# Performance work log

Measured on AMD Instinct MI355X. Metric: run time of the kernel, lower is better.

## Reference

```python
import jax, jax.numpy as jnp
import numpy as np

N = 50000       # num nodes
F_NODE = 8      # node_features
T_IN = 8        # num_timestamps_in (A3TGCN periods)
T_OUT = 4       # num_timestamps_out
HID = 16        # A3TGCN out_channels (hard-coded in module)
E = 800000      # num edges


def setup_inputs() -> dict:
    key = jax.random.key(0)
    ks = jax.random.split(key, 12)
    f32 = jnp.float32
    x = jax.random.normal(ks[0], (N, F_NODE, T_IN), dtype=f32)
    edge_index = jax.random.randint(ks[1], (2, E), 0, N)

    def w(k, shape):
        return (jax.random.normal(k, shape, dtype=f32) * 0.1)

    return {
        "x": x,
        "edge_index": edge_index,
        "attention": w(ks[2], (T_IN,)),
        "Wz": w(ks[3], (F_NODE, HID)), "bz": jnp.zeros((HID,), f32),
        "Lz_w": w(ks[4], (2 * HID, HID)), "Lz_b": jnp.zeros((HID,), f32),
        "Wr": w(ks[5], (F_NODE, HID)), "br": jnp.zeros((HID,), f32),
        "Lr_w": w(ks[6], (2 * HID, HID)), "Lr_b": jnp.zeros((HID,), f32),
        "Wh": w(ks[7], (F_NODE, HID)), "bh": jnp.zeros((HID,), f32),
        "Lh_w": w(ks[8], (2 * HID, HID)), "Lh_b": jnp.zeros((HID,), f32),
        "W_out": w(ks[9], (HID, F_NODE)), "b_out": jnp.zeros((F_NODE,), f32),
    }


def _gcn_norms(src, dst):
    # PyG gcn_norm: add self loops (weight 1), symmetric D^-1/2 (A+I) D^-1/2
    deg = jax.ops.segment_sum(jnp.ones((E,), jnp.float32), dst, num_segments=N) + 1.0
    dinv = jax.lax.rsqrt(deg)
    return dinv[src] * dinv[dst], dinv * dinv  # per-edge norm, self-loop norm


def _gcn(X, W, b, src, dst, norm_e, norm_self):
    xw = X @ W                                        # [N, HID]
    agg = jax.ops.segment_sum(xw[src] * norm_e[:, None], dst, num_segments=N)
    return agg + norm_self[:, None] * xw + b


def reference(x, edge_index, attention,
              Wz, bz, Lz_w, Lz_b,
              Wr, br, Lr_w, Lr_b,
              Wh, bh, Lh_w, Lh_b,
              W_out, b_out):
    src, dst = edge_index[0], edge_index[1]
    norm_e, norm_self = _gcn_norms(src, dst)
    probs = jax.nn.softmax(attention)                 # attention over periods

    def tgcn_cell(Xp, H):
        # GRU with GCNConv-based gates (TGCN)
        Z = jax.nn.sigmoid(
            jnp.concatenate([_gcn(Xp, Wz, bz, src, dst, norm_e, norm_self), H], axis=1) @ Lz_w + Lz_b)
        R = jax.nn.sigmoid(
            jnp.concatenate([_gcn(Xp, Wr, br, src, dst, norm_e, norm_self), H], axis=1) @ Lr_w + Lr_b)
        H_t = jnp.tanh(
            jnp.concatenate([_gcn(Xp, Wh, bh, src, dst, norm_e, norm_self), H * R], axis=1) @ Lh_w + Lh_b)
        return Z * H + (1.0 - Z) * H_t

    def a3tgcn(x_cur):
        xs = jnp.transpose(x_cur, (2, 0, 1))          # [T_IN, N, F]
        def step(carry, inp):
            H, H_acc = carry
            Xp, p = inp
            H = tgcn_cell(Xp, H)
            return (H, H_acc + p * H), None
        init = (jnp.zeros((N, HID), x_cur.dtype), jnp.zeros((N, HID), x_cur.dtype))
        (_, H_acc), _ = jax.lax.scan(step, init, (xs, probs))
        return H_acc

    outs = []
    for _ in range(T_OUT):
        h = jax.nn.relu(a3tgcn(x)) @ W_out + b_out    # [N, F]
        h = h[:, :, None]                              # [N, F, 1]
        x = jnp.concatenate([x[:, :, 1:], h], axis=2)  # slide window
        outs.append(h)
    return jnp.concatenate(outs, axis=2)               # [N, F, T_OUT]
```

## Files before the change

kernel.cpp:

```cpp
#include <hip/hip_runtime.h>

#define NN 50000
#define NE 800000
#define N8 (8*NN)
#define CAP 64

__device__ __forceinline__ float sigmoidf_(float x){ return 1.0f/(1.0f+__expf(-x)); }
__device__ __forceinline__ float tanhfast_(float x){ return 1.0f - 2.0f/(__expf(2.0f*x)+1.0f); }

__global__ void k_zero_fold(int* __restrict__ cnt, const float* __restrict__ att,
    const float* __restrict__ Wz, const float* __restrict__ bz,
    const float* __restrict__ Lzw, const float* __restrict__ Lzb,
    const float* __restrict__ Wr, const float* __restrict__ br,
    const float* __restrict__ Lrw, const float* __restrict__ Lrb,
    const float* __restrict__ Wh, const float* __restrict__ bh,
    const float* __restrict__ Lhw, const float* __restrict__ Lhb,
    const float* __restrict__ Wo, const float* __restrict__ bo,
    float* __restrict__ fold){
    if(blockIdx.x < 196){
        cnt[blockIdx.x*256 + threadIdx.x] = 0;
        return;
    }
    int tid = threadIdx.x;
    const float* Ws[3]  = {Wz, Wr, Wh};
    const float* bs[3]  = {bz, br, bh};
    const float* Ls[3]  = {Lzw, Lrw, Lhw};
    const float* Lbs[3] = {Lzb, Lrb, Lhb};
    if(tid < 48){
        int g = tid >> 4, j = tid & 15;
        const float* W = Ws[g]; const float* L = Ls[g];
        float c = Lbs[g][j];
        for(int k = 0; k < 16; ++k) c += bs[g][k] * L[k*16 + j];
        fold[1280 + g*16 + j] = c;
        for(int f = 0; f < 8; ++f){
            float m = 0.f;
            for(int k = 0; k < 16; ++k) m += W[f*16 + k] * L[k*16 + j];
            fold[j*28 + g*8 + f] = m;
        }
    }
    for(int idx = tid; idx < 768; idx += 256){
        int g = idx >> 8, rr = idx & 255, i = rr >> 4, j = rr & 15;
        fold[448 + j*52 + g*16 + i] = Ls[g][(16 + i)*16 + j];
    }
    for(int idx = tid; idx < 128; idx += 256) fold[1328 + idx] = Wo[idx];
    if(tid < 8) fold[1456 + tid] = bo[tid];
    if(tid == 0){
        float mx = att[0];
        for(int k = 1; k < 8; ++k) mx = fmaxf(mx, att[k]);
        float den = 0.f, ex[8];
        for(int k = 0; k < 8; ++k){ ex[k] = __expf(att[k] - mx); den += ex[k]; }
        for(int k = 0; k < 8; ++k) fold[1464 + k] = ex[k] / den;
    }
}

__global__ void k_hist(const int* __restrict__ ei, int* __restrict__ cnt,
                       int* __restrict__ rank){
    int e = blockIdx.x*256 + threadIdx.x;
    rank[e] = atomicAdd(&cnt[ei[NE + e]], 1);
}

__global__ void k_scatter_xscale(const int* __restrict__ ei, const int* __restrict__ rank,
                                 int* __restrict__ csr, const float* __restrict__ x,
                                 const int* __restrict__ cnt, float* __restrict__ xs){
    if(blockIdx.x < 3125){
        int e = blockIdx.x*256 + threadIdx.x;
        int r = rank[e];
        if(r < CAP) csr[(size_t)ei[NE + e]*CAP + r] = ei[e];
    } else {
        int idx = (blockIdx.x - 3125)*256 + threadIdx.x;
        int n = idx >> 4;
        const float4* x4 = (const float4*)x;
        float4 v = x4[idx];
        float d = rsqrtf((float)cnt[n] + 1.0f);
        v.x *= d; v.y *= d; v.z *= d; v.w *= d;
        ((float4*)xs)[idx] = v;
    }
}

__global__ __launch_bounds__(256) void k_gather_x2(
    const int* __restrict__ cnt, const int* __restrict__ csr,
    const float* __restrict__ xs, float* __restrict__ Pall){
    int lane = threadIdx.x & 63;
    int n = blockIdx.x*4 + (threadIdx.x >> 6);
    int g = lane >> 4;
    int q = lane & 15;
    int cn = cnt[n];
    int deg = cn < CAP ? cn : CAP;
    const int* row = csr + (size_t)n*CAP;
    const float4* xs4 = (const float4*)xs;

    float4 a0, a1, a2, a3;
    if(g == 0){ a0 = xs4[(size_t)n*16 + q]; }
    else      { a0.x = a0.y = a0.z = a0.w = 0.f; }
    a1.x = a1.y = a1.z = a1.w = 0.f;
    a2 = a1; a3 = a1;

    int it = 0;
    for(; it + 16 <= deg; it += 16){
        int ka = it + g;
        int s0 = row[ka], s1 = row[ka+4], s2 = row[ka+8], s3 = row[ka+12];
        float4 v0 = xs4[(size_t)s0*16 + q];
        float4 v1 = xs4[(size_t)s1*16 + q];
        float4 v2 = xs4[(size_t)s2*16 + q];
        float4 v3 = xs4[(size_t)s3*16 + q];
        a0.x += v0.x; a0.y += v0.y; a0.z += v0.z; a0.w += v0.w;
        a1.x += v1.x; a1.y += v1.y; a1.z += v1.z; a1.w += v1.w;
        a2.x += v2.x; a2.y += v2.y; a2.z += v2.z; a2.w += v2.w;
        a3.x += v3.x; a3.y += v3.y; a3.z += v3.z; a3.w += v3.w;
    }
    for(int k = it + g; k < deg; k += 4){
        float4 v = xs4[(size_t)row[k]*16 + q];
        a0.x += v.x; a0.y += v.y; a0.z += v.z; a0.w += v.w;
    }
    a0.x += a1.x + a2.x + a3.x;
    a0.y += a1.y + a2.y + a3.y;
    a0.z += a1.z + a2.z + a3.z;
    a0.w += a1.w + a2.w + a3.w;

    a0.x += __shfl_xor(a0.x, 16); a0.y += __shfl_xor(a0.y, 16);
    a0.z += __shfl_xor(a0.z, 16); a0.w += __shfl_xor(a0.w, 16);
    a0.x += __shfl_xor(a0.x, 32); a0.y += __shfl_xor(a0.y, 32);
    a0.z += __shfl_xor(a0.z, 32); a0.w += __shfl_xor(a0.w, 32);

    if(g == 0){
        float dn = rsqrtf((float)cn + 1.0f);
        float a[4] = {a0.x, a0.y, a0.z, a0.w};
        #pragma unroll
        for(int m = 0; m < 4; ++m){
            int r = q*4 + m;
            int f = r >> 3, t = r & 7;
            Pall[(size_t)t*N8 + n*8 + f] = dn * a[m];
        }
    }
}

template<int TOUT>
__global__ __launch_bounds__(256) void k_cell_t(
    const float* __restrict__ Pall, float* __restrict__ Ph_all,
    const float* __restrict__ fold, const int* __restrict__ cnt,
    const int* __restrict__ csr, float* __restrict__ out,
    const float* __restrict__ hs_in, float* __restrict__ hs_out){
    __shared__ float s[1472];
    __shared__ float xch[256];
    for(int k = threadIdx.x; k < 1472; k += 256) s[k] = fold[k];
    __syncthreads();

    int tid = threadIdx.x;
    int j = tid & 15;
    int nb = tid & 240;
    int n = blockIdx.x*16 + (tid >> 4);
    int cn = cnt[n];
    float dn = rsqrtf((float)cn + 1.0f);

    float u7[8];
    if(TOUT > 0){
        int f = j & 7, g = j >> 3;
        int deg = cn < CAP ? cn : CAP;
        const int* row = csr + (size_t)n*CAP;
        float ga = 0.f, gb = 0.f;
        int k = g;
        for(; k + 4 <= deg; k += 4){
            ga += hs_in[row[k]*8 + f];
            gb += hs_in[row[k+2]*8 + f];
        }
        if(k < deg){ ga += hs_in[row[k]*8 + f]; k += 2; }
        if(k < deg){ gb += hs_in[row[k]*8 + f]; }
        ga += gb;
        ga += __shfl_xor(ga, 8);
        float uh = dn * (ga + hs_in[n*8 + f]);
        if(j < 8){
            xch[nb + j] = uh;
            Ph_all[(size_t)(TOUT-1)*N8 + n*8 + j] = uh;
        }
        *(float4*)&u7[0] = *(const float4*)&xch[nb + 0];
        *(float4*)&u7[4] = *(const float4*)&xch[nb + 4];
    }

    const float* Mrow = s + j*28;
    const float* Lrow = s + 448 + j*52;
    float mw[24];
    #pragma unroll
    for(int k = 0; k < 6; ++k) *(float4*)&mw[k*4] = *(const float4*)&Mrow[k*4];
    float lw[48];
    #pragma unroll
    for(int k = 0; k < 12; ++k) *(float4*)&lw[k*4] = *(const float4*)&Lrow[k*4];
    float cz = s[1280 + j], cr = s[1296 + j], ch = s[1312 + j];

    float Hown = 0.f, Acc = 0.f;

    #pragma unroll
    for(int st = 0; st < 8; ++st){
        const int t = TOUT + st;
        float u[8];
        if(TOUT > 0 && st == 7){
            #pragma unroll
            for(int f = 0; f < 8; ++f) u[f] = u7[f];
        } else {
            const float* Pu = (t < 8) ? (Pall + (size_t)t*N8 + n*8)
                                      : (Ph_all + (size_t)(t - 8)*N8 + n*8);
            const float4* Pu4 = (const float4*)Pu;
            float4 b0 = Pu4[0], b1 = Pu4[1];
            u[0]=b0.x; u[1]=b0.y; u[2]=b0.z; u[3]=b0.w;
            u[4]=b1.x; u[5]=b1.y; u[6]=b1.z; u[7]=b1.w;
        }

        float Hf[16];
        xch[tid] = Hown;
        *(float4*)&Hf[0]  = *(const float4*)&xch[nb + 0];
        *(float4*)&Hf[4]  = *(const float4*)&xch[nb + 4];
        *(float4*)&Hf[8]  = *(const float4*)&xch[nb + 8];
        *(float4*)&Hf[12] = *(const float4*)&xch[nb + 12];

        float az = cz, ar = cr;
        #pragma unroll
        for(int f = 0; f < 8; ++f){ az += u[f]*mw[f]; ar += u[f]*mw[8+f]; }
        #pragma unroll
        for(int i = 0; i < 16; ++i){ az += Hf[i]*lw[i]; ar += Hf[i]*lw[16+i]; }
        float Z = sigmoidf_(az);
        float R = sigmoidf_(ar);

        float HRf[16];
        xch[tid] = Hown*R;
        *(float4*)&HRf[0]  = *(const float4*)&xch[nb + 0];
        *(float4*)&HRf[4]  = *(const float4*)&xch[nb + 4];
        *(float4*)&HRf[8]  = *(const float4*)&xch[nb + 8];
        *(float4*)&HRf[12] = *(const float4*)&xch[nb + 12];

        float ah = ch;
        #pragma unroll
        for(int f = 0; f < 8; ++f) ah += u[f]*mw[16+f];
        #pragma unroll
        for(int i = 0; i < 16; ++i) ah += HRf[i]*lw[32+i];
        float ht = tanhfast_(ah);
        Hown = Z*Hown + (1.0f - Z)*ht;
        Acc += s[1464 + st]*Hown;
    }

    float rf[16];
    xch[tid] = Acc > 0.f ? Acc : 0.f;
    *(float4*)&rf[0]  = *(const float4*)&xch[nb + 0];
    *(float4*)&rf[4]  = *(const float4*)&xch[nb + 4];
    *(float4*)&rf[8]  = *(const float4*)&xch[nb + 8];
    *(float4*)&rf[12] = *(const float4*)&xch[nb + 12];
    if(j < 8){
        int f = j;
        float o = s[1456 + f];
        #pragma unroll
        for(int jj = 0; jj < 16; ++jj) o += rf[jj] * s[1328 + jj*8 + f];
        out[(size_t)n*32 + f*4 + TOUT] = o;
        if(TOUT < 3) hs_out[n*8 + f] = dn * o;
    }
}

extern "C" void kernel_launch(void* const* d_in, const int* in_sizes, int n_in,
                              void* d_out, int out_size, void* d_ws, size_t ws_size,
                              hipStream_t stream){
    const float* x   = (const float*)d_in[0];
    const int*   ei  = (const int*)  d_in[1];
    const float* att = (const float*)d_in[2];
    const float* Wz  = (const float*)d_in[3];  const float* bz  = (const float*)d_in[4];
    const float* Lzw = (const float*)d_in[5];  const float* Lzb = (const float*)d_in[6];
    const float* Wr  = (const float*)d_in[7];  const float* br  = (const float*)d_in[8];
    const float* Lrw = (const float*)d_in[9];  const float* Lrb = (const float*)d_in[10];
    const float* Wh  = (const float*)d_in[11]; const float* bh  = (const float*)d_in[12];
    const float* Lhw = (const float*)d_in[13]; const float* Lhb = (const float*)d_in[14];
    const float* Wo  = (const float*)d_in[15]; const float* bo  = (const float*)d_in[16];
    float* out = (float*)d_out;

    char* w = (char*)d_ws;
    int*   cnt  = (int*)  (w);
    int*   csr  = (int*)  (w + (size_t)50176*4);
    float* fold = (float*)(w + (size_t)3250176*4);
    float* xs   = (float*)(w + (size_t)3251712*4);
    float* Pall = (float*)(w + (size_t)6451712*4);
    int*   rank = (int*)Pall;
    float* Ph   = xs;
    float* hs0  = xs + 1200000;
    float* hs1  = xs + 1600000;

    dim3 b(256);
    k_zero_fold<<<197, b, 0, stream>>>(cnt, att, Wz, bz, Lzw, Lzb, Wr, br, Lrw, Lrb,
                                       Wh, bh, Lhw, Lhb, Wo, bo, fold);
    k_hist<<<3125, b, 0, stream>>>(ei, cnt, rank);
    k_scatter_xscale<<<6250, b, 0, stream>>>(ei, rank, csr, x, cnt, xs);
    k_gather_x2<<<12500, b, 0, stream>>>(cnt, csr, xs, Pall);

    k_cell_t<0><<<3125, b, 0, stream>>>(Pall, Ph, fold, cnt, csr, out, hs1, hs0);
    k_cell_t<1><<<3125, b, 0, stream>>>(Pall, Ph, fold, cnt, csr, out, hs0, hs1);
    k_cell_t<2><<<3125, b, 0, stream>>>(Pall, Ph, fold, cnt, csr, out, hs1, hs0);
    k_cell_t<3><<<3125, b, 0, stream>>>(Pall, Ph, fold, cnt, csr, out, hs0, hs1);
}
```

Baseline: 312.8 us.

## Process two nodes per thread group in GRU cell kernel and fuse CSR build

The cell kernel now handles two nodes per 16-lane group, so each loaded weight is reused across both nodes and the number of blocks is halved. The H exchange through shared memory packs both nodes as float2. Separately, the histogram and CSR scatter are merged into one atomic-rank-and-write kernel, and the x scaling gets its own launch, which drops the rank array round trip. In exchange the cell kernel uses more registers, which may lower occupancy, and the fused build makes the CSR slot order depend on atomic timing.

```diff
diff --git a/kernel.cpp b/kernel.cpp
--- a/kernel.cpp
+++ b/kernel.cpp
@@ -53,28 +53,23 @@
     }
 }
 
-__global__ void k_hist(const int* __restrict__ ei, int* __restrict__ cnt,
-                       int* __restrict__ rank){
+__global__ void k_build(const int* __restrict__ ei, int* __restrict__ cnt,
+                        int* __restrict__ csr){
     int e = blockIdx.x*256 + threadIdx.x;
-    rank[e] = atomicAdd(&cnt[ei[NE + e]], 1);
-}
-
-__global__ void k_scatter_xscale(const int* __restrict__ ei, const int* __restrict__ rank,
-                                 int* __restrict__ csr, const float* __restrict__ x,
-                                 const int* __restrict__ cnt, float* __restrict__ xs){
-    if(blockIdx.x < 3125){
-        int e = blockIdx.x*256 + threadIdx.x;
-        int r = rank[e];
-        if(r < CAP) csr[(size_t)ei[NE + e]*CAP + r] = ei[e];
-    } else {
-        int idx = (blockIdx.x - 3125)*256 + threadIdx.x;
-        int n = idx >> 4;
-        const float4* x4 = (const float4*)x;
-        float4 v = x4[idx];
-        float d = rsqrtf((float)cnt[n] + 1.0f);
-        v.x *= d; v.y *= d; v.z *= d; v.w *= d;
-        ((float4*)xs)[idx] = v;
-    }
+    int s = ei[e], d = ei[NE + e];
+    int r = atomicAdd(&cnt[d], 1);
+    if(r < CAP) csr[(size_t)d*CAP + r] = s;
+}
+
+__global__ void k_xscale(const float* __restrict__ x, const int* __restrict__ cnt,
+                         float* __restrict__ xs){
+    int idx = blockIdx.x*256 + threadIdx.x;
+    int n = idx >> 4;
+    const float4* x4 = (const float4*)x;
+    float4 v = x4[idx];
+    float d = rsqrtf((float)cnt[n] + 1.0f);
+    v.x *= d; v.y *= d; v.z *= d; v.w *= d;
+    ((float4*)xs)[idx] = v;
 }
 
 __global__ __launch_bounds__(256) void k_gather_x2(
@@ -141,39 +136,56 @@
     const int* __restrict__ csr, float* __restrict__ out,
     const float* __restrict__ hs_in, float* __restrict__ hs_out){
     __shared__ float s[1472];
-    __shared__ float xch[256];
+    __shared__ float xch[16*36];
     for(int k = threadIdx.x; k < 1472; k += 256) s[k] = fold[k];
     __syncthreads();
 
     int tid = threadIdx.x;
     int j = tid & 15;
-    int nb = tid & 240;
-    int n = blockIdx.x*16 + (tid >> 4);
-    int cn = cnt[n];
-    float dn = rsqrtf((float)cn + 1.0f);
-
-    float u7[8];
+    int grp = tid >> 4;
+    float2* xb = (float2*)&xch[grp*36];
+    const float4* xb4 = (const float4*)xb;
+    int n0 = blockIdx.x*32 + grp;
+    int n1 = n0 + 16;
+    bool v1 = (n1 < NN);
+    int n1c = v1 ? n1 : NN-1;
+    int c0 = cnt[n0], c1 = cnt[n1c];
+    float dn0 = rsqrtf((float)c0 + 1.f), dn1 = rsqrtf((float)c1 + 1.f);
+
+    float u7x[8], u7y[8];
     if(TOUT > 0){
-        int f = j & 7, g = j >> 3;
-        int deg = cn < CAP ? cn : CAP;
-        const int* row = csr + (size_t)n*CAP;
-        float ga = 0.f, gb = 0.f;
-        int k = g;
-        for(; k + 4 <= deg; k += 4){
-            ga += hs_in[row[k]*8 + f];
-            gb += hs_in[row[k+2]*8 + f];
-        }
-        if(k < deg){ ga += hs_in[row[k]*8 + f]; k += 2; }
-        if(k < deg){ gb += hs_in[row[k]*8 + f]; }
-        ga += gb;
-        ga += __shfl_xor(ga, 8);
-        float uh = dn * (ga + hs_in[n*8 + f]);
+        int f = j & 7, g2 = j >> 3;
+        int d0 = c0 < CAP ? c0 : CAP;
+        int d1 = c1 < CAP ? c1 : CAP;
+        const int* r0 = csr + (size_t)n0*CAP;
+        const int* r1 = csr + (size_t)n1c*CAP;
+        float a0 = 0.f, b0 = 0.f, a1 = 0.f, b1 = 0.f;
+        int k = g2;
+        for(; k + 4 <= d0; k += 4){
+            a0 += hs_in[r0[k]*8 + f];
+            b0 += hs_in[r0[k+2]*8 + f];
+        }
+        if(k < d0){ a0 += hs_in[r0[k]*8 + f]; k += 2; }
+        if(k < d0){ b0 += hs_in[r0[k]*8 + f]; }
+        k = g2;
+        for(; k + 4 <= d1; k += 4){
+            a1 += hs_in[r1[k]*8 + f];
+            b1 += hs_in[r1[k+2]*8 + f];
+        }
+        if(k < d1){ a1 += hs_in[r1[k]*8 + f]; k += 2; }
+        if(k < d1){ b1 += hs_in[r1[k]*8 + f]; }
+        a0 += b0; a1 += b1;
+        a0 += __shfl_xor(a0, 8);
+        a1 += __shfl_xor(a1, 8);
+        float uh0 = dn0*(a0 + hs_in[n0*8 + f]);
+        float uh1 = dn1*(a1 + hs_in[n1c*8 + f]);
         if(j < 8){
-            xch[nb + j] = uh;
-            Ph_all[(size_t)(TOUT-1)*N8 + n*8 + j] = uh;
-        }
-        *(float4*)&u7[0] = *(const float4*)&xch[nb + 0];
-        *(float4*)&u7[4] = *(const float4*)&xch[nb + 4];
+            xb[j] = make_float2(uh0, uh1);
+            Ph_all[(size_t)(TOUT-1)*N8 + n0*8 + j] = uh0;
+            if(v1) Ph_all[(size_t)(TOUT-1)*N8 + n1*8 + j] = uh1;
+        }
+        #pragma unroll
+        for(int ff = 0; ff < 8; ++ff){ float2 t2 = xb[ff]; u7x[ff] = t2.x; u7y[ff] = t2.y; }
     }
 
     const float* Mrow = s + j*28;
@@ -186,69 +198,78 @@
     for(int k = 0; k < 12; ++k) *(float4*)&lw[k*4] = *(const float4*)&Lrow[k*4];
     float cz = s[1280 + j], cr = s[1296 + j], ch = s[1312 + j];
 
-    float Hown = 0.f, Acc = 0.f;
+    float2 H = make_float2(0.f, 0.f), Acc = make_float2(0.f, 0.f);
 
     #pragma unroll
     for(int st = 0; st < 8; ++st){
         const int t = TOUT + st;
-        float u[8];
+        float ux[8], uy[8];
         if(TOUT > 0 && st == 7){
             #pragma unroll
-            for(int f = 0; f < 8; ++f) u[f] = u7[f];
+            for(int f = 0; f < 8; ++f){ ux[f] = u7x[f]; uy[f] = u7y[f]; }
         } else {
-            const float* Pu = (t < 8) ? (Pall + (size_t)t*N8 + n*8)
-                                      : (Ph_all + (size_t)(t - 8)*N8 + n*8);
-            const float4* Pu4 = (const float4*)Pu;
-            float4 b0 = Pu4[0], b1 = Pu4[1];
-            u[0]=b0.x; u[1]=b0.y; u[2]=b0.z; u[3]=b0.w;
-            u[4]=b1.x; u[5]=b1.y; u[6]=b1.z; u[7]=b1.w;
-        }
-
-        float Hf[16];
-        xch[tid] = Hown;
-        *(float4*)&Hf[0]  = *(const float4*)&xch[nb + 0];
-        *(float4*)&Hf[4]  = *(const float4*)&xch[nb + 4];
-        *(float4*)&Hf[8]  = *(const float4*)&xch[nb + 8];
-        *(float4*)&Hf[12] = *(const float4*)&xch[nb + 12];
-
-        float az = cz, ar = cr;
-        #pragma unroll
-        for(int f = 0; f < 8; ++f){ az += u[f]*mw[f]; ar += u[f]*mw[8+f]; }
-        #pragma unroll
-        for(int i = 0; i < 16; ++i){ az += Hf[i]*lw[i]; ar += Hf[i]*lw[16+i]; }
-        float Z = sigmoidf_(az);
-        float R = sigmoidf_(ar);
-
-        float HRf[16];
-        xch[tid] = Hown*R;
-        *(float4*)&HRf[0]  = *(const float4*)&xch[nb + 0];
-        *(float4*)&HRf[4]  = *(const float4*)&xch[nb + 4];
-        *(float4*)&HRf[8]  = *(const float4*)&xch[nb + 8];
-        *(float4*)&HRf[12] = *(const float4*)&xch[nb + 12];
-
-        float ah = ch;
-        #pragma unroll
-        for(int f = 0; f < 8; ++f) ah += u[f]*mw[16+f];
-        #pragma unroll
-        for(int i = 0; i < 16; ++i) ah += HRf[i]*lw[32+i];
-        float ht = tanhfast_(ah);
-        Hown = Z*Hown + (1.0f - Z)*ht;
-        Acc += s[1464 + st]*Hown;
-    }
-
-    float rf[16];
-    xch[tid] = Acc > 0.f ? Acc : 0.f;
-    *(float4*)&rf[0]  = *(const float4*)&xch[nb + 0];
-    *(float4*)&rf[4]  = *(const float4*)&xch[nb + 4];
-    *(float4*)&rf[8]  = *(const float4*)&xch[nb + 8];
-    *(float4*)&rf[12] = *(const float4*)&xch[nb + 12];
+            const float* base = (t < 8) ? (Pall + (size_t)t*N8) : (Ph_all + (size_t)(t - 8)*N8);
+            const float4* p0 = (const float4*)(base + n0*8);
+            const float4* p1 = (const float4*)(base + (size_t)n1c*8);
+            float4 q0 = p0[0], q1 = p0[1], q2 = p1[0], q3 = p1[1];
+            ux[0]=q0.x; ux[1]=q0.y; ux[2]=q0.z; ux[3]=q0.w;
+            ux[4]=q1.x; ux[5]=q1.y; ux[6]=q1.z; ux[7]=q1.w;
+            uy[0]=q2.x; uy[1]=q2.y; uy[2]=q2.z; uy[3]=q2.w;
+            uy[4]=q3.x; uy[5]=q3.y; uy[6]=q3.z; uy[7]=q3.w;
+        }
+
+        float2 az = make_float2(cz, cz), ar = make_float2(cr, cr), ah = make_float2(ch, ch);
+        #pragma unroll
+        for(int f = 0; f < 8; ++f){
+            az.x += ux[f]*mw[f];    az.y += uy[f]*mw[f];
+            ar.x += ux[f]*mw[8+f];  ar.y += uy[f]*mw[8+f];
+            ah.x += ux[f]*mw[16+f]; ah.y += uy[f]*mw[16+f];
+        }
+
+        xb[j] = H;
+        #pragma unroll
+        for(int i = 0; i < 8; ++i){
+            float4 hv = xb4[i];
+            az.x += hv.x*lw[2*i];      az.y += hv.y*lw[2*i];
+            az.x += hv.z*lw[2*i+1];    az.y += hv.w*lw[2*i+1];
+            ar.x += hv.x*lw[16+2*i];   ar.y += hv.y*lw[16+2*i];
+            ar.x += hv.z*lw[16+2*i+1]; ar.y += hv.w*lw[16+2*i+1];
+        }
+        float2 Z = make_float2(sigmoidf_(az.x), sigmoidf_(az.y));
+        float2 R = make_float2(sigmoidf_(ar.x), sigmoidf_(ar.y));
+
+        xb[j] = make_float2(H.x*R.x, H.y*R.y);
+        #pragma unroll
+        for(int i = 0; i < 8; ++i){
+            float4 hv = xb4[i];
+            ah.x += hv.x*lw[32+2*i];   ah.y += hv.y*lw[32+2*i];
+            ah.x += hv.z*lw[32+2*i+1]; ah.y += hv.w*lw[32+2*i+1];
+        }
+        float2 ht = make_float2(tanhfast_(ah.x), tanhfast_(ah.y));
+        H.x = Z.x*H.x + (1.0f - Z.x)*ht.x;
+        H.y = Z.y*H.y + (1.0f - Z.y)*ht.y;
+        float p = s[1464 + st];
+        Acc.x += p*H.x; Acc.y += p*H.y;
+    }
+
+    xb[j] = make_float2(Acc.x > 0.f ? Acc.x : 0.f, Acc.y > 0.f ? Acc.y : 0.f);
     if(j < 8){
-        int f = j;
-        float o = s[1456 + f];
-        #pragma unroll
-        for(int jj = 0; jj < 16; ++jj) o += rf[jj] * s[1328 + jj*8 + f];
-        out[(size_t)n*32 + f*4 + TOUT] = o;
-        if(TOUT < 3) hs_out[n*8 + f] = dn * o;
+        float bo = s[1456 + j];
+        float2 o = make_float2(bo, bo);
+        #pragma unroll
+        for(int jj = 0; jj < 8; ++jj){
+            float4 rv = xb4[jj];
+            float w0 = s[1328 + (2*jj)*8 + j];
+            float w1 = s[1328 + (2*jj+1)*8 + j];
+            o.x += rv.x*w0; o.y += rv.y*w0;
+            o.x += rv.z*w1; o.y += rv.w*w1;
+        }
+        out[(size_t)n0*32 + j*4 + TOUT] = o.x;
+        if(v1) out[(size_t)n1*32 + j*4 + TOUT] = o.y;
+        if(TOUT < 3){
+            hs_out[n0*8 + j] = dn0*o.x;
+            if(v1) hs_out[n1*8 + j] = dn1*o.y;
+        }
     }
 }
 
@@ -273,7 +294,6 @@
     float* fold = (float*)(w + (size_t)3250176*4);
     float* xs   = (float*)(w + (size_t)3251712*4);
     float* Pall = (float*)(w + (size_t)6451712*4);
-    int*   rank = (int*)Pall;
     float* Ph   = xs;
     float* hs0  = xs + 1200000;
     float* hs1  = xs + 1600000;
@@ -281,12 +301,12 @@
     dim3 b(256);
     k_zero_fold<<<197, b, 0, stream>>>(cnt, att, Wz, bz, Lzw, Lzb, Wr, br, Lrw, Lrb,
                                        Wh, bh, Lhw, Lhb, Wo, bo, fold);
-    k_hist<<<3125, b, 0, stream>>>(ei, cnt, rank);
-    k_scatter_xscale<<<6250, b, 0, stream>>>(ei, rank, csr, x, cnt, xs);
+    k_build<<<3125, b, 0, stream>>>(ei, cnt, csr);
+    k_xscale<<<3125, b, 0, stream>>>(x, cnt, xs);
     k_gather_x2<<<12500, b, 0, stream>>>(cnt, csr, xs, Pall);
 
-    k_cell_t<0><<<3125, b, 0, stream>>>(Pall, Ph, fold, cnt, csr, out, hs1, hs0);
-    k_cell_t<1><<<3125, b, 0, stream>>>(Pall, Ph, fold, cnt, csr, out, hs0, hs1);
-    k_cell_t<2><<<3125, b, 0, stream>>>(Pall, Ph, fold, cnt, csr, out, hs1, hs0);
-    k_cell_t<3><<<3125, b, 0, stream>>>(Pall, Ph, fold, cnt, csr, out, hs0, hs1);
-}
+    k_cell_t<0><<<1563, b, 0, stream>>>(Pall, Ph, fold, cnt, csr, out, hs1, hs0);
+    k_cell_t<1><<<1563, b, 0, stream>>>(Pall, Ph, fold, cnt, csr, out, hs0, hs1);
+    k_cell_t<2><<<1563, b, 0, stream>>>(Pall, Ph, fold, cnt, csr, out, hs1, hs0);
+    k_cell_t<3><<<1563, b, 0, stream>>>(Pall, Ph, fold, cnt, csr, out, hs0, hs1);
+}
```

New measurement: 373.1 us. 19.2% more time.

## Fuse CSR histogram and scatter; prefetch all step inputs in cell kernel

Applied to the files above, without the earlier changes.

The edge histogram and CSR scatter now run in one kernel: each edge's atomicAdd result is used directly as its slot index, so the rank array no longer has to be written and read back. The x scaling moves into its own small kernel. In the cell kernel, the eight per-step input vectors are loaded into registers up front, before the neighbour gather and the recurrent loop. This lets the global loads overlap the other work, at the cost of about 64 extra registers per thread and possible occupancy pressure.

```diff
diff --git a/kernel.cpp b/kernel.cpp
--- a/kernel.cpp
+++ b/kernel.cpp
@@ -53,28 +53,23 @@
     }
 }
 
-__global__ void k_hist(const int* __restrict__ ei, int* __restrict__ cnt,
-                       int* __restrict__ rank){
+__global__ void k_build(const int* __restrict__ ei, int* __restrict__ cnt,
+                        int* __restrict__ csr){
     int e = blockIdx.x*256 + threadIdx.x;
-    rank[e] = atomicAdd(&cnt[ei[NE + e]], 1);
-}
-
-__global__ void k_scatter_xscale(const int* __restrict__ ei, const int* __restrict__ rank,
-                                 int* __restrict__ csr, const float* __restrict__ x,
-                                 const int* __restrict__ cnt, float* __restrict__ xs){
-    if(blockIdx.x < 3125){
-        int e = blockIdx.x*256 + threadIdx.x;
-        int r = rank[e];
-        if(r < CAP) csr[(size_t)ei[NE + e]*CAP + r] = ei[e];
-    } else {
-        int idx = (blockIdx.x - 3125)*256 + threadIdx.x;
-        int n = idx >> 4;
-        const float4* x4 = (const float4*)x;
-        float4 v = x4[idx];
-        float d = rsqrtf((float)cnt[n] + 1.0f);
-        v.x *= d; v.y *= d; v.z *= d; v.w *= d;
-        ((float4*)xs)[idx] = v;
-    }
+    int s = ei[e], d = ei[NE + e];
+    int r = atomicAdd(&cnt[d], 1);
+    if(r < CAP) csr[(size_t)d*CAP + r] = s;
+}
+
+__global__ void k_xscale(const float* __restrict__ x, const int* __restrict__ cnt,
+                         float* __restrict__ xs){
+    int idx = blockIdx.x*256 + threadIdx.x;
+    int n = idx >> 4;
+    const float4* x4 = (const float4*)x;
+    float4 v = x4[idx];
+    float d = rsqrtf((float)cnt[n] + 1.0f);
+    v.x *= d; v.y *= d; v.z *= d; v.w *= d;
+    ((float4*)xs)[idx] = v;
 }
 
 __global__ __launch_bounds__(256) void k_gather_x2(
@@ -152,7 +147,19 @@
     int cn = cnt[n];
     float dn = rsqrtf((float)cn + 1.0f);
 
-    float u7[8];
+    float ub[8][8];
+    #pragma unroll
+    for(int st = 0; st < 8; ++st){
+        if(TOUT > 0 && st == 7) continue;
+        const int t = TOUT + st;
+        const float* base = (t < 8) ? (Pall + (size_t)t*N8)
+                                    : (Ph_all + (size_t)(t - 8)*N8);
+        const float4* p = (const float4*)(base + (size_t)n*8);
+        float4 b0 = p[0], b1 = p[1];
+        ub[st][0]=b0.x; ub[st][1]=b0.y; ub[st][2]=b0.z; ub[st][3]=b0.w;
+        ub[st][4]=b1.x; ub[st][5]=b1.y; ub[st][6]=b1.z; ub[st][7]=b1.w;
+    }
+
     if(TOUT > 0){
         int f = j & 7, g = j >> 3;
         int deg = cn < CAP ? cn : CAP;
@@ -172,8 +179,8 @@
             xch[nb + j] = uh;
             Ph_all[(size_t)(TOUT-1)*N8 + n*8 + j] = uh;
         }
-        *(float4*)&u7[0] = *(const float4*)&xch[nb + 0];
-        *(float4*)&u7[4] = *(const float4*)&xch[nb + 4];
+        *(float4*)&ub[7][0] = *(const float4*)&xch[nb + 0];
+        *(float4*)&ub[7][4] = *(const float4*)&xch[nb + 4];
     }
 
     const float* Mrow = s + j*28;
@@ -190,19 +197,7 @@
 
     #pragma unroll
     for(int st = 0; st < 8; ++st){
-        const int t = TOUT + st;
-        float u[8];
-        if(TOUT > 0 && st == 7){
-            #pragma unroll
-            for(int f = 0; f < 8; ++f) u[f] = u7[f];
-        } else {
-            const float* Pu = (t < 8) ? (Pall + (size_t)t*N8 + n*8)
-                                      : (Ph_all + (size_t)(t - 8)*N8 + n*8);
-            const float4* Pu4 = (const float4*)Pu;
-            float4 b0 = Pu4[0], b1 = Pu4[1];
-            u[0]=b0.x; u[1]=b0.y; u[2]=b0.z; u[3]=b0.w;
-            u[4]=b1.x; u[5]=b1.y; u[6]=b1.z; u[7]=b1.w;
-        }
+        const float* u = ub[st];
 
         float Hf[16];
         xch[tid] = Hown;
@@ -273,7 +268,6 @@
     float* fold = (float*)(w + (size_t)3250176*4);
     float* xs   = (float*)(w + (size_t)3251712*4);
     float* Pall = (float*)(w + (size_t)6451712*4);
-    int*   rank = (int*)Pall;
     float* Ph   = xs;
     float* hs0  = xs + 1200000;
     float* hs1  = xs + 1600000;
@@ -281,8 +275,8 @@
     dim3 b(256);
     k_zero_fold<<<197, b, 0, stream>>>(cnt, att, Wz, bz, Lzw, Lzb, Wr, br, Lrw, Lrb,
                                        Wh, bh, Lhw, Lhb, Wo, bo, fold);
-    k_hist<<<3125, b, 0, stream>>>(ei, cnt, rank);
-    k_scatter_xscale<<<6250, b, 0, stream>>>(ei, rank, csr, x, cnt, xs);
+    k_build<<<3125, b, 0, stream>>>(ei, cnt, csr);
+    k_xscale<<<3125, b, 0, stream>>>(x, cnt, xs);
     k_gather_x2<<<12500, b, 0, stream>>>(cnt, csr, xs, Pall);
 
     k_cell_t<0><<<3125, b, 0, stream>>>(Pall, Ph, fold, cnt, csr, out, hs1, hs0);
```

Result: no change. 307.0 us (-1.8%).
